# Kernel optimization log

Measured on AMD Instinct MI355X. Metric: run time of the kernel, lower is better.

Reference implementation:

```python
import jax, jax.numpy as jnp
import numpy as np

# ---- static config (matches init_kwargs) ----
N, E = 8192, 262144
IN_CH, MP_CH, HID, K = 128, 512, 256, 10
EPS, DELTA = 1e-3, 0.311
TV_COEFF, BAL_COEFF = 0.785, 0.514


def setup_inputs() -> dict:
    key = jax.random.key(0)
    ks = jax.random.split(key, 16)

    def p(k, shape):
        fan_in = shape[0] if len(shape) > 1 else shape[0]
        return (jax.random.normal(k, shape, jnp.float32) / np.sqrt(fan_in)).astype(jnp.float32)

    return {
        "x": jax.random.normal(ks[0], (N, IN_CH), jnp.float32),
        "edge_index": jax.random.randint(ks[1], (2, E), 0, N, jnp.int32),
        "edge_weight": jax.random.uniform(ks[2], (E,), jnp.float32),
        # GTVConv layer 1 / 2 (Linear weight + bias)
        "W1": p(ks[3], (IN_CH, MP_CH)), "b1": jnp.zeros((MP_CH,), jnp.float32),
        "W2": p(ks[4], (MP_CH, MP_CH)), "b2": jnp.zeros((MP_CH,), jnp.float32),
        # pooling MLP [512 -> 256 -> K], relu, no norm
        "Wm1": p(ks[5], (MP_CH, HID)), "bm1": jnp.zeros((HID,), jnp.float32),
        "Wm2": p(ks[6], (HID, K)), "bm2": jnp.zeros((K,), jnp.float32),
    }


def _gtv_conv(x, src, dst, w, W, b):
    """GTVConv: out = elu( h - delta*(D_G h - Gamma h) + b ),
    gamma_ij = w_ij / max(||h_i - h_j||_1, eps), h = x @ W."""
    h = x @ W                                   # [N, C]
    diff = jnp.sum(jnp.abs(h[src] - h[dst]), axis=-1)   # [E]
    gamma = w / jnp.maximum(diff, EPS)                  # [E]
    deg = jnp.zeros(h.shape[0], h.dtype).at[dst].add(gamma)          # [N]
    agg = jnp.zeros_like(h).at[dst].add(gamma[:, None] * h[src])     # Gamma @ h
    out = h - DELTA * (deg[:, None] * h - agg) + b
    return jax.nn.elu(out)


def reference(x, edge_index, edge_weight, W1, b1, W2, b2, Wm1, bm1, Wm2, bm2):
    src, dst = edge_index[0], edge_index[1]

    h = _gtv_conv(x, src, dst, edge_weight, W1, b1)
    h = _gtv_conv(h, src, dst, edge_weight, W2, b2)

    # pooling MLP -> cluster logits s
    s_logits = jax.nn.relu(h @ Wm1 + bm1) @ Wm2 + bm2   # [N, K]

    # dense adjacency (to_dense_adj: duplicate edges accumulate)
    adj = jnp.zeros((N, N), x.dtype).at[src, dst].add(edge_weight)

    s = jax.nn.softmax(s_logits, axis=-1)

    # total-variation loss: sum_ij a_ij * sum_k |s_ik - s_jk| / (2 * nnz(adj))
    tv = jnp.zeros((), x.dtype)
    for k in range(K):  # small fixed loop over clusters, avoids [N,N,K] tensor
        col = s[:, k]
        tv = tv + jnp.sum(adj * jnp.abs(col[:, None] - col[None, :]))
    n_edges = jax.lax.stop_gradient(jnp.count_nonzero(adj).astype(x.dtype))
    tv = tv / (2.0 * n_edges)

    # asymmetric-norm balance loss (AsymCheegerCut)
    idx = N // K + 1                         # rho-quantile index (static)
    quant = jnp.sort(s, axis=0)[N - idx]     # idx-th largest per cluster, [K]
    t = s - quant[None, :]
    asym = jnp.where(t >= 0, (K - 1) * t, -t)
    denom = float(N * (K - 1))
    bal = (denom - jnp.sum(asym)) / denom

    return s_logits, TV_COEFF * tv, BAL_COEFF * bal
```

## Files before the change

### kernel.cpp

```cpp
#include <hip/hip_runtime.h>

#define N_NODES 8192
#define N_EDGES 262144
#define IN_CH 128
#define MP_CH 512
#define HID 256
#define KCL 10
#define EPS_C 0.001f
#define DELTA_C 0.311f
#define TV_COEFF_C 0.785f
#define BAL_COEFF_C 0.514f
#define RANK1 7373
#define DBINS 80


typedef __bf16 bf16x8 __attribute__((ext_vector_type(8)));
typedef float f32x4 __attribute__((ext_vector_type(4)));
typedef unsigned short ushort8 __attribute__((ext_vector_type(8)));

__device__ __forceinline__ float bf2f(unsigned short h) {
  union { unsigned int u; float f; } c; c.u = ((unsigned int)h) << 16; return c.f;
}
__device__ __forceinline__ unsigned short f2bf(float f) {
  union { float f; unsigned int u; } c; c.f = f;
  unsigned int r = c.u + 0x7fffu + ((c.u >> 16) & 1u);
  return (unsigned short)(r >> 16);
}

__global__ void prep_kernel(const float* __restrict__ x, const float* __restrict__ W1,
                            const float* __restrict__ W2, const float* __restrict__ Wm1,
                            unsigned short* __restrict__ xb, unsigned short* __restrict__ W1bt,
                            unsigned short* __restrict__ W2bt, unsigned short* __restrict__ Wm1bt,
                            const int* __restrict__ dst, int* __restrict__ cnt) {
  int i = blockIdx.x * 256 + threadIdx.x;
  if (i < 1048576) { xb[i] = f2bf(x[i]); return; }
  i -= 1048576;
  if (i < 65536) { int n = i >> 7, k = i & 127; W1bt[i] = f2bf(W1[k * MP_CH + n]); return; }
  i -= 65536;
  if (i < 262144) { int n = i >> 9, k = i & 511; W2bt[i] = f2bf(W2[k * MP_CH + n]); return; }
  i -= 262144;
  if (i < 131072) { int n = i >> 9, k = i & 511; Wm1bt[i] = f2bf(Wm1[k * HID + n]); return; }
  i -= 131072;
  if (i < N_EDGES) atomicAdd(&cnt[dst[i]], 1);
}

__global__ __launch_bounds__(1024) void scan_kernel(const int* __restrict__ cnt,
                                                    int* __restrict__ offs,
                                                    int* __restrict__ cursor,
                                                    int* __restrict__ nodeorder) {
  __shared__ int ts[1024];
  __shared__ int dh[DBINS];
  int t = threadIdx.x;
  int v[8]; int s = 0;
#pragma unroll
  for (int j = 0; j < 8; ++j) { v[j] = cnt[t * 8 + j]; s += v[j]; }
  if (t < DBINS) dh[t] = 0;
  ts[t] = s; __syncthreads();
  for (int off = 1; off < 1024; off <<= 1) {
    int add = (t >= off) ? ts[t - off] : 0;
    __syncthreads();
    ts[t] += add;
    __syncthreads();
  }
  int base = ts[t] - s;
#pragma unroll
  for (int j = 0; j < 8; ++j) {
    offs[t * 8 + j] = base; cursor[t * 8 + j] = base; base += v[j];
    int key = v[j] < (DBINS - 1) ? v[j] : (DBINS - 1);
    atomicAdd(&dh[(DBINS - 1) - key], 1);
  }
  if (t == 1023) offs[N_NODES] = ts[1023];
  __syncthreads();
  if (t == 0) {
    int acc0 = 0;
    for (int b = 0; b < DBINS; ++b) { int c = dh[b]; dh[b] = acc0; acc0 += c; }
  }
  __syncthreads();
#pragma unroll
  for (int j = 0; j < 8; ++j) {
    int key = v[j] < (DBINS - 1) ? v[j] : (DBINS - 1);
    int pos = atomicAdd(&dh[(DBINS - 1) - key], 1);
    nodeorder[pos] = t * 8 + j;
  }
}

__global__ void fill_kernel(const int* __restrict__ src, const int* __restrict__ dst,
                            const float* __restrict__ ew, int* __restrict__ cursor,
                            int2* __restrict__ esw) {
  for (int e = blockIdx.x * blockDim.x + threadIdx.x; e < N_EDGES; e += gridDim.x * blockDim.x) {
    int p = atomicAdd(&cursor[dst[e]], 1);
    esw[p] = make_int2(src[e], __float_as_int(ew[e]));
  }
}

__global__ __launch_bounds__(256) void gemm_bt(
    const unsigned short* __restrict__ A, const unsigned short* __restrict__ BT,
    unsigned short* __restrict__ Cb, int N, int K) {
  __shared__ unsigned short lsm[2 * 128 * 32];
  unsigned short* lA = lsm;
  unsigned short* lB = lsm + 128 * 32;
  int lane = threadIdx.x & 63;
  int wv = threadIdx.x >> 6;
  int tm = blockIdx.y * 128, tn = blockIdx.x * 128;
  int wm = (wv >> 1) * 64, wn = (wv & 1) * 64;
  int rA = lane & 15, quad = lane >> 4;
  f32x4 acc[4][4];
#pragma unroll
  for (int i = 0; i < 4; ++i)
#pragma unroll
    for (int j = 0; j < 4; ++j) acc[i][j] = (f32x4){0.f, 0.f, 0.f, 0.f};

  int arow = wv * 32 + (lane >> 2);
  int acol = (lane & 3) * 8;

  for (int k0 = 0; k0 < K; k0 += 32) {
#pragma unroll
    for (int c = 0; c < 2; ++c) {
      const unsigned short* ga = A + (size_t)(tm + arow + c * 16) * K + k0 + acol;
      __builtin_amdgcn_global_load_lds(
          (const __attribute__((address_space(1))) unsigned int*)ga,
          (__attribute__((address_space(3))) unsigned int*)(lA + (wv * 32 + c * 16) * 32),
          16, 0, 0);
      const unsigned short* gb = BT + (size_t)(tn + arow + c * 16) * K + k0 + acol;
      __builtin_amdgcn_global_load_lds(
          (const __attribute__((address_space(1))) unsigned int*)gb,
          (__attribute__((address_space(3))) unsigned int*)(lB + (wv * 32 + c * 16) * 32),
          16, 0, 0);
    }
    __syncthreads();
    bf16x8 af[4], bfr[4];
#pragma unroll
    for (int i = 0; i < 4; ++i)
      af[i] = *(const bf16x8*)(lA + (wm + i * 16 + rA) * 32 + quad * 8);
#pragma unroll
    for (int j = 0; j < 4; ++j)
      bfr[j] = *(const bf16x8*)(lB + (wn + j * 16 + rA) * 32 + quad * 8);
#pragma unroll
    for (int i = 0; i < 4; ++i)
#pragma unroll
      for (int j = 0; j < 4; ++j)
        acc[i][j] = __builtin_amdgcn_mfma_f32_16x16x32_bf16(af[i], bfr[j], acc[i][j], 0, 0, 0);
    __syncthreads();
  }

  float* fbuf = (float*)lsm;
  int band = threadIdx.x >> 7;
  int rrow = (threadIdx.x >> 3) & 15;
  int cg = threadIdx.x & 7;
#pragma unroll
  for (int i = 0; i < 4; ++i) {
#pragma unroll
    for (int j = 0; j < 4; ++j)
#pragma unroll
      for (int r = 0; r < 4; ++r)
        fbuf[(wv >> 1) * (16 * 128) + (quad * 4 + r) * 128 + (wn + j * 16 + rA)] =
            acc[i][j][r];
    __syncthreads();
    const float* sr = fbuf + band * (16 * 128) + rrow * 128 + cg * 16;
    unsigned short ov[16];
#pragma unroll
    for (int c = 0; c < 16; ++c) ov[c] = f2bf(sr[c]);
    size_t gbase = (size_t)(tm + band * 64 + i * 16 + rrow) * N + tn + cg * 16;
    *(ushort8*)(Cb + gbase) = *(ushort8*)ov;
    *(ushort8*)(Cb + gbase + 8) = *(ushort8*)(ov + 8);
    __syncthreads();
  }
}

__global__ __launch_bounds__(256, 8) void gtv_node(
    const unsigned short* __restrict__ hb, const float* __restrict__ bias,
    const int2* __restrict__ esw, const int* __restrict__ offs,
    const int* __restrict__ nodeorder, unsigned short* __restrict__ outb) {
  __shared__ float sacc[2][MP_CH];
  int lane = threadIdx.x & 63;
  int wv = threadIdx.x >> 6;
  int pair = wv >> 1;
  int half = wv & 1;
  int d = __builtin_amdgcn_readfirstlane(nodeorder[blockIdx.x * 2 + pair]);
  ushort8 hdv = ((const ushort8*)(hb + (size_t)d * MP_CH))[lane];
  float hd[8], acc[8];
#pragma unroll
  for (int j = 0; j < 8; ++j) { hd[j] = bf2f(hdv[j]); acc[j] = 0.f; }
  int n0 = offs[d], n1 = offs[d + 1];
  int mid = n0 + ((n1 - n0 + 1) >> 1);
  int e0 = half ? mid : n0;
  int e1 = half ? n1 : mid;
  int i = e0;
  for (; i + 1 < e1; i += 2) {
    int2 ma = esw[i], mb = esw[i + 1];
    float wa = __int_as_float(ma.y), wb = __int_as_float(mb.y);
    ushort8 va = ((const ushort8*)(hb + (size_t)ma.x * MP_CH))[lane];
    ushort8 vb = ((const ushort8*)(hb + (size_t)mb.x * MP_CH))[lane];
    float pa = 0.f, pb = 0.f;
#pragma unroll
    for (int j = 0; j < 8; ++j) {
      pa += fabsf(hd[j] - bf2f(va[j]));
      pb += fabsf(hd[j] - bf2f(vb[j]));
    }
#pragma unroll
    for (int m = 1; m < 64; m <<= 1) { pa += __shfl_xor(pa, m, 64); pb += __shfl_xor(pb, m, 64); }
    float ga = wa * __builtin_amdgcn_rcpf(fmaxf(pa, EPS_C));
    float gb = wb * __builtin_amdgcn_rcpf(fmaxf(pb, EPS_C));
#pragma unroll
    for (int j = 0; j < 8; ++j)
      acc[j] += ga * (hd[j] - bf2f(va[j])) + gb * (hd[j] - bf2f(vb[j]));
  }
  if (i < e1) {
    int2 m0 = esw[i];
    float w = __int_as_float(m0.y);
    ushort8 sv = ((const ushort8*)(hb + (size_t)m0.x * MP_CH))[lane];
    float part = 0.f;
#pragma unroll
    for (int j = 0; j < 8; ++j) part += fabsf(hd[j] - bf2f(sv[j]));
#pragma unroll
    for (int m = 1; m < 64; m <<= 1) part += __shfl_xor(part, m, 64);
    float g = w * __builtin_amdgcn_rcpf(fmaxf(part, EPS_C));
#pragma unroll
    for (int j = 0; j < 8; ++j) acc[j] += g * (hd[j] - bf2f(sv[j]));
  }
  if (half) {
#pragma unroll
    for (int j = 0; j < 8; ++j) sacc[pair][lane * 8 + j] = acc[j];
  }
  __syncthreads();
  if (!half) {
    const f32x4* br = (const f32x4*)(bias + lane * 8);
    f32x4 b0 = br[0], b1 = br[1];
    unsigned short ov[8];
#pragma unroll
    for (int j = 0; j < 8; ++j) {
      float tot = acc[j] + sacc[pair][lane * 8 + j];
      float bv = (j < 4) ? b0[j] : b1[j - 4];
      float o = hd[j] - DELTA_C * tot + bv;
      o = (o > 0.f) ? o : (expf(o) - 1.f);
      ov[j] = f2bf(o);
    }
    *((ushort8*)(outb + (size_t)d * MP_CH) + lane) = *(ushort8*)ov;
  }
}

__global__ __launch_bounds__(256) void head_fused(
    const unsigned short* __restrict__ A,
    const unsigned short* __restrict__ BT,
    const float* __restrict__ bm1v, const float* __restrict__ Wm2v,
    const float* __restrict__ bm2v, float* __restrict__ out, float* __restrict__ s) {
  __shared__ unsigned short lA[32 * 32];
  __shared__ unsigned short lB[256 * 32];
  __shared__ float hbuf[256 * 41];
  __shared__ float lW2[HID * KCL];
  __shared__ float lb1[HID];
  __shared__ float lb2[KCL];
  int t = threadIdx.x;
  int lane = t & 63, wv = t >> 6;
  int rA = lane & 15, quad = lane >> 4;
  int m0 = blockIdx.x * 32;

  for (int i2 = t; i2 < HID * KCL; i2 += 256) lW2[i2] = Wm2v[i2];
  lb1[t < HID ? t : 0] = bm1v[t < HID ? t : 0];
  if (t < KCL) lb2[t] = bm2v[t];

  f32x4 acc[2][4];
#pragma unroll
  for (int i = 0; i < 2; ++i)
#pragma unroll
    for (int j = 0; j < 4; ++j) acc[i][j] = (f32x4){0.f, 0.f, 0.f, 0.f};

  for (int k0 = 0; k0 < MP_CH; k0 += 32) {
    if (wv < 2) {
      int row = wv * 16 + (lane >> 2);
      const unsigned short* ga = A + (size_t)(m0 + row) * MP_CH + k0 + (lane & 3) * 8;
      __builtin_amdgcn_global_load_lds(
          (const __attribute__((address_space(1))) unsigned int*)ga,
          (__attribute__((address_space(3))) unsigned int*)(lA + (wv * 16) * 32), 16, 0, 0);
    }
#pragma unroll
    for (int q = 0; q < 4; ++q) {
      int idx = wv * 4 + q;
      int row = idx * 16 + (lane >> 2);
      const unsigned short* gb = BT + (size_t)row * MP_CH + k0 + (lane & 3) * 8;
      __builtin_amdgcn_global_load_lds(
          (const __attribute__((address_space(1))) unsigned int*)gb,
          (__attribute__((address_space(3))) unsigned int*)(lB + (idx * 16) * 32), 16, 0, 0);
    }
    __syncthreads();
    bf16x8 af[2], bfr[4];
#pragma unroll
    for (int i = 0; i < 2; ++i)
      af[i] = *(const bf16x8*)(lA + (i * 16 + rA) * 32 + quad * 8);
#pragma unroll
    for (int j = 0; j < 4; ++j)
      bfr[j] = *(const bf16x8*)(lB + (wv * 64 + j * 16 + rA) * 32 + quad * 8);
#pragma unroll
    for (int i = 0; i < 2; ++i)
#pragma unroll
      for (int j = 0; j < 4; ++j)
        acc[i][j] = __builtin_amdgcn_mfma_f32_16x16x32_bf16(af[i], bfr[j], acc[i][j], 0, 0, 0);
    __syncthreads();
  }

#pragma unroll
  for (int i = 0; i < 2; ++i)
#pragma unroll
    for (int j = 0; j < 4; ++j)
#pragma unroll
      for (int r = 0; r < 4; ++r) {
        int row = i * 16 + quad * 4 + r;
        int col = wv * 64 + j * 16 + rA;
        hbuf[col * 41 + row] = fmaxf(acc[i][j][r] + lb1[col], 0.f);
      }
  __syncthreads();

  int row = t >> 3, g = t & 7;
  float p[KCL];
#pragma unroll
  for (int n = 0; n < KCL; ++n) p[n] = 0.f;
#pragma unroll
  for (int k = 0; k < 32; ++k) {
    int col = k * 8 + g;
    float hv = hbuf[col * 41 + row];
    const float* wr = lW2 + col * KCL;
#pragma unroll
    for (int n = 0; n < KCL; ++n) p[n] += hv * wr[n];
  }
#pragma unroll
  for (int n = 0; n < KCL; ++n) {
    p[n] += __shfl_xor(p[n], 1, 64);
    p[n] += __shfl_xor(p[n], 2, 64);
    p[n] += __shfl_xor(p[n], 4, 64);
  }
  if (g == 0) {
    float vv[KCL]; float mx = -1e30f;
    size_t gr = (size_t)(m0 + row);
#pragma unroll
    for (int n = 0; n < KCL; ++n) {
      vv[n] = p[n] + lb2[n];
      out[gr * KCL + n] = vv[n];
      mx = fmaxf(mx, vv[n]);
    }
    float sum = 0.f;
#pragma unroll
    for (int n = 0; n < KCL; ++n) { vv[n] = expf(vv[n] - mx); sum += vv[n]; }
    float inv = 1.f / sum;
#pragma unroll
    for (int n = 0; n < KCL; ++n) s[gr * KCL + n] = vv[n] * inv;
  }
}

__global__ __launch_bounds__(1024) void tvquant_kernel(
    const int* __restrict__ src, const int* __restrict__ dst,
    const float* __restrict__ ew, const float* __restrict__ s,
    unsigned int* __restrict__ bitmap, float* __restrict__ scal) {
  __shared__ float fsh[16];
  __shared__ int wcnt[2][16];
  int t = threadIdx.x;
  int lane = t & 63, wv = t >> 6;
  if (blockIdx.x < 246) {
    float local = 0.f;
    for (int e = blockIdx.x * 1024 + t; e < N_EDGES; e += 246 * 1024) {
      int a = src[e], b = dst[e];
      float w = ew[e];
      const float* sa = s + (size_t)a * KCL;
      const float* sb = s + (size_t)b * KCL;
      float tv = 0.f;
#pragma unroll
      for (int k = 0; k < KCL; ++k) tv += fabsf(sa[k] - sb[k]);
      local += w * tv;
      if (w != 0.f) {
        unsigned int key = ((unsigned int)a << 13) | (unsigned int)b;
        atomicOr(&bitmap[key >> 5], 1u << (key & 31u));
      }
    }
#pragma unroll
    for (int m = 1; m < 64; m <<= 1) local += __shfl_xor(local, m, 64);
    if (lane == 0) fsh[wv] = local;
    __syncthreads();
    if (t == 0) {
      float tot = 0.f;
#pragma unroll
      for (int i2 = 0; i2 < 16; ++i2) tot += fsh[i2];
      atomicAdd(&scal[0], tot);
    }
  } else {
    int k = blockIdx.x - 246;
    unsigned int v[8];
#pragma unroll
    for (int j = 0; j < 8; ++j)
      v[j] = __float_as_uint(s[(size_t)(t + j * 1024) * KCL + k]);
    unsigned int lo = 0u, hi = 0x3F800000u;
    int p = 0;
    while (lo < hi) {
      unsigned int mid = (lo + hi) >> 1;
      int c = 0;
#pragma unroll
      for (int j = 0; j < 8; ++j) c += (v[j] <= mid) ? 1 : 0;
#pragma unroll
      for (int m = 1; m < 64; m <<= 1) c += __shfl_xor(c, m, 64);
      if (lane == 0) wcnt[p][wv] = c;
      __syncthreads();
      int tot = 0;
#pragma unroll
      for (int i2 = 0; i2 < 16; ++i2) tot += wcnt[p][i2];
      if (tot >= RANK1) hi = mid; else lo = mid + 1;
      p ^= 1;
    }
    float q = __uint_as_float(lo);
    float local = 0.f;
#pragma unroll
    for (int j = 0; j < 8; ++j) {
      float tt = __uint_as_float(v[j]) - q;
      local += (tt >= 0.f) ? 9.f * tt : -tt;
    }
#pragma unroll
    for (int m = 1; m < 64; m <<= 1) local += __shfl_xor(local, m, 64);
    if (lane == 0) fsh[wv] = local;
    __syncthreads();
    if (t == 0) {
      float tot = 0.f;
#pragma unroll
      for (int i2 = 0; i2 < 16; ++i2) tot += fsh[i2];
      atomicAdd(&scal[1], tot);
    }
  }
}

__global__ __launch_bounds__(1024) void popcfin_kernel(const unsigned int* __restrict__ bm,
                                                       float* __restrict__ scal,
                                                       float* __restrict__ out) {
  __shared__ int ish[16];
  int t = threadIdx.x;
  int lane = t & 63, wv = t >> 6;
  int local = 0;
  for (int i = blockIdx.x * 1024 + t; i < (1 << 21); i += 256 * 1024)
    local += __popc(bm[i]);
#pragma unroll
  for (int m = 1; m < 64; m <<= 1) local += __shfl_xor(local, m, 64);
  if (lane == 0) ish[wv] = local;
  __syncthreads();
  if (t == 0) {
    int tot = 0;
#pragma unroll
    for (int i2 = 0; i2 < 16; ++i2) tot += ish[i2];
    atomicAdd((int*)(scal + 2), tot);
    __threadfence();
    int d = atomicAdd((int*)(scal + 3), 1);
    if (d == 255) {
      float tv = scal[0], asym = scal[1];
      float nedges = (float)(*(int*)(scal + 2));
      out[N_NODES * KCL] = TV_COEFF_C * (tv / (2.f * nedges));
      out[N_NODES * KCL + 1] = BAL_COEFF_C * ((73728.f - asym) / 73728.f);
    }
  }
}

#define OFF_BM     ((size_t)0)
#define OFF_CNT    ((size_t)8388608)
#define OFF_SCAL   ((size_t)8421376)
#define OFF_OFFS   ((size_t)8421888)
#define OFF_CURSOR ((size_t)8454912)
#define OFF_NORD   ((size_t)8487936)
#define OFF_HB     ((size_t)16777216)
#define OFF_OUTB   ((size_t)25165824)
#define OFF_ESW    ((size_t)33554432)
#define OFF_XB     ((size_t)41943040)
#define OFF_W1BT   ((size_t)44040192)
#define OFF_W2BT   ((size_t)44171264)
#define OFF_WM1BT  ((size_t)44695552)
#define OFF_S      ((size_t)44957696)

extern "C" void kernel_launch(void* const* d_in, const int* in_sizes, int n_in,
                              void* d_out, int out_size, void* d_ws, size_t ws_size,
                              hipStream_t stream) {
  const float* x   = (const float*)d_in[0];
  const int*   ei  = (const int*)d_in[1];
  const float* ew  = (const float*)d_in[2];
  const float* W1  = (const float*)d_in[3];
  const float* b1  = (const float*)d_in[4];
  const float* W2  = (const float*)d_in[5];
  const float* b2  = (const float*)d_in[6];
  const float* Wm1 = (const float*)d_in[7];
  const float* bm1 = (const float*)d_in[8];
  const float* Wm2 = (const float*)d_in[9];
  const float* bm2 = (const float*)d_in[10];
  float* out = (float*)d_out;

  char* ws = (char*)d_ws;
  unsigned int*   bitmap = (unsigned int*)(ws + OFF_BM);
  int*            cnt    = (int*)(ws + OFF_CNT);
  float*          scal   = (float*)(ws + OFF_SCAL);
  int*            offs   = (int*)(ws + OFF_OFFS);
  int*            cursor = (int*)(ws + OFF_CURSOR);
  int*            nord   = (int*)(ws + OFF_NORD);
  unsigned short* hb     = (unsigned short*)(ws + OFF_HB);
  unsigned short* outb   = (unsigned short*)(ws + OFF_OUTB);
  int2*           esw    = (int2*)(ws + OFF_ESW);
  unsigned short* xb     = (unsigned short*)(ws + OFF_XB);
  unsigned short* W1bt   = (unsigned short*)(ws + OFF_W1BT);
  unsigned short* W2bt   = (unsigned short*)(ws + OFF_W2BT);
  unsigned short* Wm1bt  = (unsigned short*)(ws + OFF_WM1BT);
  float*          s      = (float*)(ws + OFF_S);

  const int* srcA = ei;
  const int* dstA = ei + N_EDGES;

  hipMemsetAsync(ws, 0, 8421632, stream);

  prep_kernel<<<6912, 256, 0, stream>>>(x, W1, W2, Wm1, xb, W1bt, W2bt, Wm1bt, dstA, cnt);
  scan_kernel<<<1, 1024, 0, stream>>>(cnt, offs, cursor, nord);
  fill_kernel<<<1024, 256, 0, stream>>>(srcA, dstA, ew, cursor, esw);

  gemm_bt<<<dim3(MP_CH / 128, N_NODES / 128), 256, 0, stream>>>(xb, W1bt, hb, MP_CH, IN_CH);
  gtv_node<<<N_NODES / 2, 256, 0, stream>>>(hb, b1, esw, offs, nord, outb);
  gemm_bt<<<dim3(MP_CH / 128, N_NODES / 128), 256, 0, stream>>>(outb, W2bt, hb, MP_CH, MP_CH);
  gtv_node<<<N_NODES / 2, 256, 0, stream>>>(hb, b2, esw, offs, nord, outb);
  head_fused<<<N_NODES / 32, 256, 0, stream>>>(outb, Wm1bt, bm1, Wm2, bm2, out, s);

  tvquant_kernel<<<256, 1024, 0, stream>>>(srcA, dstA, ew, s, bitmap, scal);
  popcfin_kernel<<<256, 1024, 0, stream>>>(bitmap, scal, out);
}
```

Before: 251.5 us.

## Move bitmap build into fill kernel, fuse popcount into tvquant, vectorize prep

The adjacency bitmap atomicOr moves from the TV kernel into the edge fill kernel, and the popcount/finalize kernel is folded into tvquant, with each block popcounting its own 8192-word slice of the bitmap. The last block to finish then writes the loss scalars. The prep kernel now converts 8 elements per thread with vector stores, and the launch grid shrinks to match. This removes one kernel launch and one pass over the edges, and it shortens the serial tail. In exchange, the fill kernel now does more atomic work, and the finalize step depends on a cross-block counter read through atomics.

Measured after the change: 255.8 us. Within noise of the previous version (+1.7%).

```diff
diff --git a/kernel.cpp b/kernel.cpp
--- a/kernel.cpp
+++ b/kernel.cpp
@@ -33,14 +33,43 @@
                             unsigned short* __restrict__ W2bt, unsigned short* __restrict__ Wm1bt,
                             const int* __restrict__ dst, int* __restrict__ cnt) {
   int i = blockIdx.x * 256 + threadIdx.x;
-  if (i < 1048576) { xb[i] = f2bf(x[i]); return; }
-  i -= 1048576;
-  if (i < 65536) { int n = i >> 7, k = i & 127; W1bt[i] = f2bf(W1[k * MP_CH + n]); return; }
-  i -= 65536;
-  if (i < 262144) { int n = i >> 9, k = i & 511; W2bt[i] = f2bf(W2[k * MP_CH + n]); return; }
-  i -= 262144;
-  if (i < 131072) { int n = i >> 9, k = i & 511; Wm1bt[i] = f2bf(Wm1[k * HID + n]); return; }
+  if (i < 131072) {
+    f32x4 a = *(const f32x4*)(x + (size_t)i * 8);
+    f32x4 b = *(const f32x4*)(x + (size_t)i * 8 + 4);
+    ushort8 ov;
+#pragma unroll
+    for (int j = 0; j < 4; ++j) { ov[j] = f2bf(a[j]); ov[4 + j] = f2bf(b[j]); }
+    *(ushort8*)(xb + (size_t)i * 8) = ov;
+    return;
+  }
   i -= 131072;
+  if (i < 8192) {
+    int n = i >> 4, kb = (i & 15) * 8;
+    ushort8 ov;
+#pragma unroll
+    for (int r = 0; r < 8; ++r) ov[r] = f2bf(W1[(size_t)(kb + r) * MP_CH + n]);
+    *(ushort8*)(W1bt + (size_t)i * 8) = ov;
+    return;
+  }
+  i -= 8192;
+  if (i < 32768) {
+    int n = i >> 6, kb = (i & 63) * 8;
+    ushort8 ov;
+#pragma unroll
+    for (int r = 0; r < 8; ++r) ov[r] = f2bf(W2[(size_t)(kb + r) * MP_CH + n]);
+    *(ushort8*)(W2bt + (size_t)i * 8) = ov;
+    return;
+  }
+  i -= 32768;
+  if (i < 16384) {
+    int n = i >> 6, kb = (i & 63) * 8;
+    ushort8 ov;
+#pragma unroll
+    for (int r = 0; r < 8; ++r) ov[r] = f2bf(Wm1[(size_t)(kb + r) * HID + n]);
+    *(ushort8*)(Wm1bt + (size_t)i * 8) = ov;
+    return;
+  }
+  i -= 16384;
   if (i < N_EDGES) atomicAdd(&cnt[dst[i]], 1);
 }
 
@@ -86,10 +115,16 @@
 
 __global__ void fill_kernel(const int* __restrict__ src, const int* __restrict__ dst,
                             const float* __restrict__ ew, int* __restrict__ cursor,
-                            int2* __restrict__ esw) {
+                            int2* __restrict__ esw, unsigned int* __restrict__ bitmap) {
   for (int e = blockIdx.x * blockDim.x + threadIdx.x; e < N_EDGES; e += gridDim.x * blockDim.x) {
-    int p = atomicAdd(&cursor[dst[e]], 1);
-    esw[p] = make_int2(src[e], __float_as_int(ew[e]));
+    int a = src[e], b = dst[e];
+    float w = ew[e];
+    int p = atomicAdd(&cursor[b], 1);
+    esw[p] = make_int2(a, __float_as_int(w));
+    if (w != 0.f) {
+      unsigned int key = ((unsigned int)a << 13) | (unsigned int)b;
+      atomicOr(&bitmap[key >> 5], 1u << (key & 31u));
+    }
   }
 }
 
@@ -349,11 +384,22 @@
 __global__ __launch_bounds__(1024) void tvquant_kernel(
     const int* __restrict__ src, const int* __restrict__ dst,
     const float* __restrict__ ew, const float* __restrict__ s,
-    unsigned int* __restrict__ bitmap, float* __restrict__ scal) {
+    const unsigned int* __restrict__ bitmap, float* __restrict__ scal,
+    float* __restrict__ out) {
   __shared__ float fsh[16];
   __shared__ int wcnt[2][16];
+  __shared__ int psh[16];
   int t = threadIdx.x;
   int lane = t & 63, wv = t >> 6;
+
+  int local_pc = 0;
+  {
+    const uint4* bm4 = (const uint4*)(bitmap + (size_t)blockIdx.x * 8192);
+    uint4 w0 = bm4[t * 2], w1 = bm4[t * 2 + 1];
+    local_pc = __popc(w0.x) + __popc(w0.y) + __popc(w0.z) + __popc(w0.w) +
+               __popc(w1.x) + __popc(w1.y) + __popc(w1.z) + __popc(w1.w);
+  }
+
   if (blockIdx.x < 246) {
     float local = 0.f;
     for (int e = blockIdx.x * 1024 + t; e < N_EDGES; e += 246 * 1024) {
@@ -365,10 +411,6 @@
 #pragma unroll
       for (int k = 0; k < KCL; ++k) tv += fabsf(sa[k] - sb[k]);
       local += w * tv;
-      if (w != 0.f) {
-        unsigned int key = ((unsigned int)a << 13) | (unsigned int)b;
-        atomicOr(&bitmap[key >> 5], 1u << (key & 31u));
-      }
     }
 #pragma unroll
     for (int m = 1; m < 64; m <<= 1) local += __shfl_xor(local, m, 64);
@@ -421,32 +463,23 @@
       atomicAdd(&scal[1], tot);
     }
   }
-}
-
-__global__ __launch_bounds__(1024) void popcfin_kernel(const unsigned int* __restrict__ bm,
-                                                       float* __restrict__ scal,
-                                                       float* __restrict__ out) {
-  __shared__ int ish[16];
-  int t = threadIdx.x;
-  int lane = t & 63, wv = t >> 6;
-  int local = 0;
-  for (int i = blockIdx.x * 1024 + t; i < (1 << 21); i += 256 * 1024)
-    local += __popc(bm[i]);
-#pragma unroll
-  for (int m = 1; m < 64; m <<= 1) local += __shfl_xor(local, m, 64);
-  if (lane == 0) ish[wv] = local;
+
+#pragma unroll
+  for (int m = 1; m < 64; m <<= 1) local_pc += __shfl_xor(local_pc, m, 64);
+  if (lane == 0) psh[wv] = local_pc;
   __syncthreads();
   if (t == 0) {
     int tot = 0;
 #pragma unroll
-    for (int i2 = 0; i2 < 16; ++i2) tot += ish[i2];
+    for (int i2 = 0; i2 < 16; ++i2) tot += psh[i2];
     atomicAdd((int*)(scal + 2), tot);
     __threadfence();
-    int d = atomicAdd((int*)(scal + 3), 1);
-    if (d == 255) {
-      float tv = scal[0], asym = scal[1];
-      float nedges = (float)(*(int*)(scal + 2));
-      out[N_NODES * KCL] = TV_COEFF_C * (tv / (2.f * nedges));
+    int dn = atomicAdd((int*)(scal + 3), 1);
+    if (dn == 255) {
+      float tv = atomicAdd(&scal[0], 0.f);
+      float asym = atomicAdd(&scal[1], 0.f);
+      int ne = atomicAdd((int*)(scal + 2), 0);
+      out[N_NODES * KCL] = TV_COEFF_C * (tv / (2.f * (float)ne));
       out[N_NODES * KCL + 1] = BAL_COEFF_C * ((73728.f - asym) / 73728.f);
     }
   }
@@ -504,9 +537,9 @@
 
   hipMemsetAsync(ws, 0, 8421632, stream);
 
-  prep_kernel<<<6912, 256, 0, stream>>>(x, W1, W2, Wm1, xb, W1bt, W2bt, Wm1bt, dstA, cnt);
+  prep_kernel<<<1760, 256, 0, stream>>>(x, W1, W2, Wm1, xb, W1bt, W2bt, Wm1bt, dstA, cnt);
   scan_kernel<<<1, 1024, 0, stream>>>(cnt, offs, cursor, nord);
-  fill_kernel<<<1024, 256, 0, stream>>>(srcA, dstA, ew, cursor, esw);
+  fill_kernel<<<1024, 256, 0, stream>>>(srcA, dstA, ew, cursor, esw, bitmap);
 
   gemm_bt<<<dim3(MP_CH / 128, N_NODES / 128), 256, 0, stream>>>(xb, W1bt, hb, MP_CH, IN_CH);
   gtv_node<<<N_NODES / 2, 256, 0, stream>>>(hb, b1, esw, offs, nord, outb);
@@ -514,6 +547,5 @@
   gtv_node<<<N_NODES / 2, 256, 0, stream>>>(hb, b2, esw, offs, nord, outb);
   head_fused<<<N_NODES / 32, 256, 0, stream>>>(outb, Wm1bt, bm1, Wm2, bm2, out, s);
 
-  tvquant_kernel<<<256, 1024, 0, stream>>>(srcA, dstA, ew, s, bitmap, scal);
-  popcfin_kernel<<<256, 1024, 0, stream>>>(bitmap, scal, out);
-}
+  tvquant_kernel<<<256, 1024, 0, stream>>>(srcA, dstA, ew, s, bitmap, scal, out);
+}
```
